# Kernel tuning notes

Hardware: AMD Instinct MI355X
Metric: run time of the kernel (lower is better)

Reference implementation:

```python
import jax, jax.numpy as jnp
import numpy as np

B, S, D = 2, 512, 1024
H, DH = 16, 64
P, K, F = 16, 4, 4096
EPS = 1e-6


def setup_inputs() -> dict:
    key = jax.random.key(0)
    ks = jax.random.split(key, 9)
    sc = D ** -0.5
    return {
        "x": jax.random.normal(ks[0], (B, S, D), jnp.float32),
        "wq": jax.random.normal(ks[1], (D, D), jnp.float32) * sc,
        "wk": jax.random.normal(ks[2], (D, D), jnp.float32) * sc,
        "wv": jax.random.normal(ks[3], (D, D), jnp.float32) * sc,
        "wo": jax.random.normal(ks[4], (D, D), jnp.float32) * sc,
        "g1": jnp.ones((D,), jnp.float32),
        "g2": jnp.ones((D,), jnp.float32),
        "r1": jax.random.normal(ks[5], (D, P), jnp.float32) * sc,
        "r2": jax.random.normal(ks[6], (D, P), jnp.float32) * sc,
        "bank1": jax.random.normal(ks[7], (P, D, F), jnp.float32) * 0.02,
        "bank2": jax.random.normal(ks[8], (P, F, D), jnp.float32) * 0.02,
    }


def _rmsnorm(t, g):
    return t * jax.lax.rsqrt(jnp.mean(t * t, axis=-1, keepdims=True) + EPS) * g


def reference(x, wq, wk, wv, wo, g1, g2, r1, r2, bank1, bank2):
    # --- attention sublayer (pre-norm, causal SDPA) ---
    h = _rmsnorm(x, g1)
    q = (h @ wq).reshape(B, S, H, DH).transpose(0, 2, 1, 3)  # (B,H,S,DH)
    k = (h @ wk).reshape(B, S, H, DH).transpose(0, 2, 1, 3)
    v = (h @ wv).reshape(B, S, H, DH).transpose(0, 2, 1, 3)
    scores = jnp.einsum("bhqd,bhkd->bhqk", q, k) * (DH ** -0.5)
    causal = jnp.triu(jnp.ones((S, S), bool), k=1)
    scores = jnp.where(causal[None, None], jnp.finfo(scores.dtype).min, scores)
    attn = jax.nn.softmax(scores, axis=-1)
    o = jnp.einsum("bhqk,bhkd->bhqd", attn, v).transpose(0, 2, 1, 3).reshape(B, S, D)
    x = x + o @ wo

    # --- compositional FFN: top-k primitive-bank routing ---
    h = _rmsnorm(x, g2)
    # FC1 routing
    tv1, ti1 = jax.lax.top_k(h @ r1, K)            # (B,S,K)
    c1 = jax.nn.softmax(tv1, axis=-1)
    z1 = jnp.einsum("bsd,pdf->bspf", h, bank1)     # all-primitive FC1 projections
    z1k = jnp.take_along_axis(z1, ti1[..., None], axis=2)  # gather (B,S,K,F)
    hmid = jax.nn.gelu(jnp.einsum("bsk,bskf->bsf", c1, z1k))
    # FC2 routing (same pre-FFN features)
    tv2, ti2 = jax.lax.top_k(h @ r2, K)
    c2 = jax.nn.softmax(tv2, axis=-1)
    z2 = jnp.einsum("bsf,pfd->bspd", hmid, bank2)
    z2k = jnp.take_along_axis(z2, ti2[..., None], axis=2)  # (B,S,K,D)
    ffn_out = jnp.einsum("bsk,bskd->bsd", c2, z2k)
    return x + ffn_out
```

## Files before the change

### kernel.cpp

```cpp
#include <hip/hip_runtime.h>
#include <hip/hip_bf16.h>

#define B_  2
#define S_  512
#define D_  1024
#define H_  16
#define DH_ 64
#define P_  16
#define K_  4
#define F_  4096
#define NT  (B_*S_)
#define EPS_ 1e-6f

typedef __attribute__((ext_vector_type(8))) short bf16x8s;
typedef __attribute__((ext_vector_type(4))) float f32x4;

__device__ inline unsigned short f2bf(float f) {
    unsigned int u = __builtin_bit_cast(unsigned int, f);
    unsigned int r = (u + 0x7fffu + ((u >> 16) & 1u)) >> 16;
    return (unsigned short)r;
}

__global__ void rmsnorm_kernel(const float* __restrict__ x, const float* __restrict__ g,
                               float* __restrict__ out, __hip_bfloat16* __restrict__ outbf) {
    int t = blockIdx.x;
    const float* row = x + (size_t)t * D_;
    float ss = 0.f;
    for (int d = threadIdx.x; d < D_; d += 256) { float v = row[d]; ss += v * v; }
    __shared__ float red[4];
    for (int off = 32; off; off >>= 1) ss += __shfl_xor(ss, off);
    int w = threadIdx.x >> 6;
    if ((threadIdx.x & 63) == 0) red[w] = ss;
    __syncthreads();
    if (threadIdx.x == 0) red[0] = rsqrtf((red[0]+red[1]+red[2]+red[3]) / (float)D_ + EPS_);
    __syncthreads();
    float scale = red[0];
    for (int d = threadIdx.x; d < D_; d += 256) {
        float v = row[d] * scale * g[d];
        out[(size_t)t * D_ + d] = v;
        if (outbf) outbf[(size_t)t * D_ + d] = __float2bfloat16(v);
    }
}

template<bool RES>
__device__ __forceinline__
void gemm64_body(const float* __restrict__ A, const float* __restrict__ Bw,
                 const float* __restrict__ Res, float* __restrict__ C,
                 int N, int Kd, int m0, int n0,
                 float (*As)[64], float (*Bs)[64]) {
    int t = threadIdx.x;
    int tx = t & 15, ty = t >> 4;
    float acc[4][4] = {};
    for (int k0 = 0; k0 < Kd; k0 += 16) {
        #pragma unroll
        for (int i = 0; i < 4; i++) {
            int idx = t*4 + i; int m = idx >> 4, kk = idx & 15;
            As[kk][m] = A[(size_t)(m0+m)*Kd + k0 + kk];
        }
        #pragma unroll
        for (int i = 0; i < 4; i++) {
            int idx = t*4 + i; int n = idx & 63, kk = idx >> 6;
            Bs[kk][n] = Bw[(size_t)(k0+kk)*N + n0 + n];
        }
        __syncthreads();
        #pragma unroll
        for (int kk = 0; kk < 16; kk++) {
            float a[4], b[4];
            #pragma unroll
            for (int i = 0; i < 4; i++) a[i] = As[kk][ty*4+i];
            #pragma unroll
            for (int j = 0; j < 4; j++) b[j] = Bs[kk][tx*4+j];
            #pragma unroll
            for (int i = 0; i < 4; i++)
                #pragma unroll
                for (int j = 0; j < 4; j++) acc[i][j] += a[i]*b[j];
        }
        __syncthreads();
    }
    #pragma unroll
    for (int i = 0; i < 4; i++)
        #pragma unroll
        for (int j = 0; j < 4; j++) {
            int m = m0 + ty*4 + i, n = n0 + tx*4 + j;
            float v = acc[i][j];
            if (RES) v += Res[(size_t)m*N + n];
            C[(size_t)m*N + n] = v;
        }
}

template<bool RES>
__global__ void gemm64(const float* __restrict__ A, const float* __restrict__ Bw,
                       const float* __restrict__ Res, float* __restrict__ C,
                       int M, int N, int Kd) {
    __shared__ float As[16][64];
    __shared__ float Bs[16][64];
    gemm64_body<RES>(A, Bw, Res, C, N, Kd, blockIdx.y*64, blockIdx.x*64, As, Bs);
}

__global__ void qkv64(const float* __restrict__ A, const float* __restrict__ wq,
                      const float* __restrict__ wk, const float* __restrict__ wv,
                      float* __restrict__ qb, float* __restrict__ kb, float* __restrict__ vb) {
    __shared__ float As[16][64];
    __shared__ float Bs[16][64];
    int which = blockIdx.x >> 4;
    const float* Bw = (which == 0) ? wq : (which == 1) ? wk : wv;
    float* C = (which == 0) ? qb : (which == 1) ? kb : vb;
    gemm64_body<false>(A, Bw, nullptr, C, D_, D_, blockIdx.y*64, (blockIdx.x & 15)*64, As, Bs);
}

template<bool SPLIT>
__global__ __launch_bounds__(256, 3)
void attn3(const float* __restrict__ q, const float* __restrict__ k,
           const float* __restrict__ v, float* __restrict__ o,
           float* __restrict__ opart, float* __restrict__ mpart,
           float* __restrict__ lpart) {
    __shared__ float Qs[32][68];
    __shared__ float Ks[64][68];
    __shared__ float Vs[64][68];
    __shared__ float Ps[32][68];
    int bh = blockIdx.y;
    int bq0 = (bh >> 4) * S_;
    int hh = bh & 15;
    int qt = blockIdx.x, q0 = qt * 32;
    int z = SPLIT ? blockIdx.z : 0;
    int t = threadIdx.x;
    int tx = t & 15, ty = t >> 4;

    #pragma unroll
    for (int i = 0; i < 2; i++) {
        int idx = i*256 + t; int r = idx >> 4, c = idx & 15;
        float4 tmp = *(const float4*)&q[((size_t)(bq0 + q0 + r))*D_ + hh*64 + c*4];
        tmp.x *= 0.125f; tmp.y *= 0.125f; tmp.z *= 0.125f; tmp.w *= 0.125f;
        *(float4*)&Qs[r][c*4] = tmp;
    }
    float m[2], l[2], oacc[2][4];
    #pragma unroll
    for (int i = 0; i < 2; i++) {
        m[i] = -1e30f; l[i] = 0.f;
        #pragma unroll
        for (int jd = 0; jd < 4; jd++) oacc[i][jd] = 0.f;
    }
    __syncthreads();

    int ktmax = (q0 + 31) >> 6;
    for (int kt = z; kt <= ktmax; kt += (SPLIT ? 2 : 1)) {
        int j0 = kt * 64;
        __syncthreads();
        #pragma unroll
        for (int i = 0; i < 4; i++) {
            int idx = i*256 + t; int r = idx >> 4, c = idx & 15;
            *(float4*)&Ks[r][c*4] = *(const float4*)&k[((size_t)(bq0 + j0 + r))*D_ + hh*64 + c*4];
            *(float4*)&Vs[r][c*4] = *(const float4*)&v[((size_t)(bq0 + j0 + r))*D_ + hh*64 + c*4];
        }
        __syncthreads();

        float sacc[2][4] = {};
        #pragma unroll
        for (int dc = 0; dc < 16; dc++) {
            f32x4 qv[2], kv[4];
            #pragma unroll
            for (int i = 0; i < 2; i++) qv[i] = *(const f32x4*)&Qs[ty + 16*i][dc*4];
            #pragma unroll
            for (int j = 0; j < 4; j++) kv[j] = *(const f32x4*)&Ks[tx + 16*j][dc*4];
            #pragma unroll
            for (int i = 0; i < 2; i++)
                #pragma unroll
                for (int j = 0; j < 4; j++)
                    sacc[i][j] += qv[i][0]*kv[j][0] + qv[i][1]*kv[j][1]
                                + qv[i][2]*kv[j][2] + qv[i][3]*kv[j][3];
        }
        if (kt == ktmax) {
            #pragma unroll
            for (int i = 0; i < 2; i++)
                #pragma unroll
                for (int j = 0; j < 4; j++)
                    if (j0 + tx + 16*j > q0 + ty + 16*i) sacc[i][j] = -1e30f;
        }
        #pragma unroll
        for (int i = 0; i < 2; i++) {
            float tm = fmaxf(fmaxf(sacc[i][0], sacc[i][1]), fmaxf(sacc[i][2], sacc[i][3]));
            tm = fmaxf(tm, __shfl_xor(tm, 1));
            tm = fmaxf(tm, __shfl_xor(tm, 2));
            tm = fmaxf(tm, __shfl_xor(tm, 4));
            tm = fmaxf(tm, __shfl_xor(tm, 8));
            float mn = fmaxf(m[i], tm);
            float corr = __expf(m[i] - mn);
            m[i] = mn;
            float rs = 0.f;
            #pragma unroll
            for (int j = 0; j < 4; j++) { sacc[i][j] = __expf(sacc[i][j] - mn); rs += sacc[i][j]; }
            rs += __shfl_xor(rs, 1);
            rs += __shfl_xor(rs, 2);
            rs += __shfl_xor(rs, 4);
            rs += __shfl_xor(rs, 8);
            l[i] = l[i]*corr + rs;
            #pragma unroll
            for (int jd = 0; jd < 4; jd++) oacc[i][jd] *= corr;
        }
        #pragma unroll
        for (int i = 0; i < 2; i++)
            #pragma unroll
            for (int j = 0; j < 4; j++)
                Ps[ty + 16*i][tx + 16*j] = sacc[i][j];
        __syncthreads();
        #pragma unroll
        for (int jc = 0; jc < 16; jc++) {
            f32x4 pv4[2];
            #pragma unroll
            for (int i = 0; i < 2; i++) pv4[i] = *(const f32x4*)&Ps[ty + 16*i][jc*4];
            #pragma unroll
            for (int u = 0; u < 4; u++) {
                int j = jc*4 + u;
                float vv[4];
                #pragma unroll
                for (int jd = 0; jd < 4; jd++) vv[jd] = Vs[j][tx + 16*jd];
                #pragma unroll
                for (int i = 0; i < 2; i++)
                    #pragma unroll
                    for (int jd = 0; jd < 4; jd++) oacc[i][jd] += pv4[i][u] * vv[jd];
            }
        }
    }
    if (SPLIT) {
        int zb = z*32 + bh;
        #pragma unroll
        for (int i = 0; i < 2; i++) {
            int row = q0 + ty + 16*i;
            if (tx == 0) {
                mpart[(size_t)zb*S_ + row] = m[i];
                lpart[(size_t)zb*S_ + row] = l[i];
            }
            #pragma unroll
            for (int jd = 0; jd < 4; jd++)
                opart[((size_t)zb*S_ + row)*64 + tx + 16*jd] = oacc[i][jd];
        }
    } else {
        #pragma unroll
        for (int i = 0; i < 2; i++) {
            float inv = 1.f / l[i];
            #pragma unroll
            for (int jd = 0; jd < 4; jd++)
                o[((size_t)(bq0 + q0 + ty + 16*i))*D_ + hh*64 + tx + 16*jd] = oacc[i][jd] * inv;
        }
    }
}

__global__ void attn_merge(const float* __restrict__ opart, const float* __restrict__ mpart,
                           const float* __restrict__ lpart, float* __restrict__ o) {
    int i = blockIdx.x*256 + threadIdx.x;
    if (i >= 32*S_*64) return;
    int col = i & 63, q = (i >> 6) & (S_-1), bh = i >> 15;
    float m0 = mpart[(size_t)bh*S_ + q],      m1 = mpart[(size_t)(32+bh)*S_ + q];
    float l0 = lpart[(size_t)bh*S_ + q],      l1 = lpart[(size_t)(32+bh)*S_ + q];
    float M = fmaxf(m0, m1);
    float w0 = __expf(m0 - M), w1 = __expf(m1 - M);
    float L = l0*w0 + l1*w1;
    float v = (opart[((size_t)bh*S_ + q)*64 + col]*w0
             + opart[((size_t)(32+bh)*S_ + q)*64 + col]*w1) / L;
    int bq0 = (bh >> 4)*S_, hh = bh & 15;
    o[((size_t)(bq0 + q))*D_ + hh*64 + col] = v;
}

__device__ void topk_write(const float* vals, float* c, int* ti) {
    float v[P_];
    #pragma unroll
    for (int p = 0; p < P_; p++) v[p] = vals[p];
    int idx[K_]; float tv[K_];
    for (int kk = 0; kk < K_; kk++) {
        int bi = 0; float bv = -1e30f;
        for (int p = 0; p < P_; p++) if (v[p] > bv) { bv = v[p]; bi = p; }
        idx[kk] = bi; tv[kk] = bv; v[bi] = -1e30f;
    }
    float mx = tv[0], sum = 0.f, e[K_];
    for (int kk = 0; kk < K_; kk++) { e[kk] = __expf(tv[kk]-mx); sum += e[kk]; }
    for (int kk = 0; kk < K_; kk++) { c[kk] = e[kk]/sum; ti[kk] = idx[kk]; }
}

__global__ void routing_kernel(const float* __restrict__ h, const float* __restrict__ r1,
                               const float* __restrict__ r2,
                               float* c1, int* ti1, float* c2, int* ti2) {
    int t = blockIdx.x; int lane = threadIdx.x;
    float acc1[P_] = {}, acc2[P_] = {};
    for (int d = lane; d < D_; d += 64) {
        float x = h[(size_t)t*D_ + d];
        #pragma unroll
        for (int p = 0; p < P_; p++) {
            acc1[p] += x * r1[d*P_ + p];
            acc2[p] += x * r2[d*P_ + p];
        }
    }
    #pragma unroll
    for (int p = 0; p < P_; p++)
        for (int off = 32; off; off >>= 1) {
            acc1[p] += __shfl_xor(acc1[p], off);
            acc2[p] += __shfl_xor(acc2[p], off);
        }
    if (lane == 0) {
        topk_write(acc1, c1 + t*K_, ti1 + t*K_);
        topk_write(acc2, c2 + t*K_, ti2 + t*K_);
    }
}

__global__ void build_lists(const int* __restrict__ ti1, const int* __restrict__ ti2,
                            int* cnt1, int* list1, int* cnt2, int* list2) {
    int slot = blockIdx.x*256 + threadIdx.x;
    if (slot >= NT*K_) return;
    int p1 = ti1[slot]; int pos1 = atomicAdd(&cnt1[p1], 1); list1[p1*(NT*K_) + pos1] = slot;
    int p2 = ti2[slot]; int pos2 = atomicAdd(&cnt2[p2], 1); list2[p2*(NT*K_) + pos2] = slot;
}

__device__ inline void store_out(__hip_bfloat16* p, float v) { *p = __float2bfloat16(v); }
__device__ inline void store_out(float* p, float v)          { *p = v; }

template<typename OutT, int KSPLIT>
__global__ __launch_bounds__(256)
void mgemm7(const __hip_bfloat16* __restrict__ A, const float* __restrict__ Bw0,
            const int* __restrict__ cnt, const int* __restrict__ list,
            OutT* __restrict__ o0, OutT* __restrict__ o1,
            OutT* __restrict__ o2, OutT* __restrict__ o3,
            int Kd, int Nd, int ntn) {
    __shared__ unsigned short Asl[4*128*8];
    __shared__ unsigned short Bsl[4*128*8];
    __shared__ int rows_s[128];
    __shared__ int slots_s[128];
    int p  = blockIdx.x / ntn;
    int n0 = (blockIdx.x - p*ntn) * 128;
    int m0 = blockIdx.y * 128;
    int count = cnt[p];
    if (m0 >= count) return;
    int t = threadIdx.x;
    if (t < 128) {
        int si = m0 + t;
        int slot = (si < count) ? list[p*(NT*K_) + si] : -1;
        slots_s[t] = slot;
        rows_s[t] = (slot >= 0) ? (slot >> 2) : 0;
    }
    __syncthreads();
    const float* Bw = Bw0 + (size_t)p * (size_t)Kd * Nd;
    int z = (KSPLIT > 1) ? (int)blockIdx.z : 0;
    OutT* out = (z == 0) ? o0 : (z == 1) ? o1 : (z == 2) ? o2 : o3;
    int kbase = z * (Kd / KSPLIT);
    int kend  = kbase + Kd / KSPLIT;
    int lane = t & 63, wave = t >> 6;
    int wr = wave >> 1, wc = wave & 1;
    int l15 = lane & 15, l4 = lane >> 4;
    int ar0 = t >> 2, ac8 = t & 3;
    int bkg = t & 7, bcg = t >> 3;
    f32x4 acc[4][4];
    #pragma unroll
    for (int i = 0; i < 4; i++)
        #pragma unroll
        for (int j = 0; j < 4; j++) acc[i][j] = (f32x4){0.f,0.f,0.f,0.f};
    int atok0 = rows_s[ar0], atok1 = rows_s[64 + ar0];
    for (int k0 = kbase; k0 < kend; k0 += 32) {
        __syncthreads();
        {
            bf16x8s av0 = *(const bf16x8s*)&A[(size_t)atok0*Kd + k0 + ac8*8];
            bf16x8s av1 = *(const bf16x8s*)&A[(size_t)atok1*Kd + k0 + ac8*8];
            *(bf16x8s*)&Asl[ac8*1024 + ((ar0 ^ (ac8<<1)) * 8)] = av0;
            *(bf16x8s*)&Asl[ac8*1024 + (((64 + ar0) ^ (ac8<<1)) * 8)] = av1;
        }
        {
            float bvv[4][4];
            #pragma unroll
            for (int j = 0; j < 4; j++) {
                float4 tmp = *(const float4*)&Bw[(size_t)(k0 + bkg*4 + j)*Nd + n0 + bcg*4];
                bvv[j][0]=tmp.x; bvv[j][1]=tmp.y; bvv[j][2]=tmp.z; bvv[j][3]=tmp.w;
            }
            int g = bkg >> 1, ib = (bkg & 1) * 4;
            #pragma unroll
            for (int cc = 0; cc < 4; cc++) {
                int col = bcg*4 + cc;
                ushort4 u = make_ushort4(f2bf(bvv[0][cc]), f2bf(bvv[1][cc]),
                                         f2bf(bvv[2][cc]), f2bf(bvv[3][cc]));
                *(ushort4*)&Bsl[g*1024 + ((col ^ (g<<1)) * 8) + ib] = u;
            }
        }
        __syncthreads();
        bf16x8s af[4], bfr[4];
        #pragma unroll
        for (int m = 0; m < 4; m++) {
            int row = wr*64 + m*16 + l15;
            af[m] = *(const bf16x8s*)&Asl[l4*1024 + ((row ^ (l4<<1)) * 8)];
        }
        #pragma unroll
        for (int n = 0; n < 4; n++) {
            int col = wc*64 + n*16 + l15;
            bfr[n] = *(const bf16x8s*)&Bsl[l4*1024 + ((col ^ (l4<<1)) * 8)];
        }
        #pragma unroll
        for (int m = 0; m < 4; m++)
            #pragma unroll
            for (int n = 0; n < 4; n++)
                acc[m][n] = __builtin_amdgcn_mfma_f32_16x16x32_bf16(af[m], bfr[n], acc[m][n], 0, 0, 0);
    }
    #pragma unroll
    for (int m = 0; m < 4; m++) {
        #pragma unroll
        for (int rr = 0; rr < 4; rr++) {
            int rl = wr*64 + m*16 + l4*4 + rr;
            int slot = slots_s[rl];
            if (slot < 0) continue;
            OutT* orow = out + (size_t)slot*Nd + n0 + wc*64;
            #pragma unroll
            for (int n = 0; n < 4; n++)
                store_out(&orow[n*16 + l15], acc[m][n][rr]);
        }
    }
}

template<bool TWO>
__global__ void reduce_fc1(const __hip_bfloat16* __restrict__ z1kA,
                           const __hip_bfloat16* __restrict__ z1kB,
                           const float* __restrict__ c1, __hip_bfloat16* __restrict__ hmid) {
    int i = blockIdx.x*256 + threadIdx.x;
    if (i >= NT*F_) return;
    int t = i / F_, f = i - t*F_;
    float s = 0.f;
    #pragma unroll
    for (int kk = 0; kk < K_; kk++) {
        size_t off = (size_t)(t*K_ + kk)*F_ + f;
        float zv = __bfloat162float(z1kA[off]);
        if (TWO) zv += __bfloat162float(z1kB[off]);
        s += c1[t*K_ + kk] * zv;
    }
    float x3 = s*s*s;
    float inner = 0.7978845608028654f * (s + 0.044715f * x3);
    hmid[i] = __float2bfloat16(0.5f * s * (1.f + tanhf(inner)));
}

template<int NP>
__global__ void final_kernel(const float* __restrict__ x2, const float* __restrict__ z0,
                             const float* __restrict__ z1, const float* __restrict__ z2p,
                             const float* __restrict__ z3,
                             const float* __restrict__ c2, float* __restrict__ out) {
    int i = blockIdx.x*256 + threadIdx.x;
    if (i >= NT*D_) return;
    int t = i / D_, d = i - t*D_;
    float s = x2[i];
    #pragma unroll
    for (int kk = 0; kk < K_; kk++) {
        size_t off = (size_t)(t*K_ + kk)*D_ + d;
        float zv = z0[off];
        if (NP >= 2) zv += z1[off];
        if (NP >= 4) zv += z2p[off] + z3[off];
        s += c2[t*K_ + kk] * zv;
    }
    out[i] = s;
}

extern "C" void kernel_launch(void* const* d_in, const int* in_sizes, int n_in,
                              void* d_out, int out_size, void* d_ws, size_t ws_size,
                              hipStream_t stream) {
    const float* x  = (const float*)d_in[0];
    const float* wq = (const float*)d_in[1];
    const float* wk = (const float*)d_in[2];
    const float* wv = (const float*)d_in[3];
    const float* wo = (const float*)d_in[4];
    const float* g1 = (const float*)d_in[5];
    const float* g2 = (const float*)d_in[6];
    const float* r1 = (const float*)d_in[7];
    const float* r2 = (const float*)d_in[8];
    const float* bank1 = (const float*)d_in[9];
    const float* bank2 = (const float*)d_in[10];
    float* out = (float*)d_out;

    char* ws = (char*)d_ws;
    const size_t MB = 1ull << 20;
    float* h1   = (float*)(ws + 0*MB);
    float* qb   = (float*)(ws + 4*MB);
    float* kb   = (float*)(ws + 8*MB);
    float* vb   = (float*)(ws + 12*MB);
    float* ob   = (float*)(ws + 16*MB);
    float* x2   = (float*)(ws + 20*MB);
    float* h2   = (float*)(ws + 24*MB);
    float* c1   = (float*)(ws + 28*MB);
    int*   ti1  = (int*)  (ws + 28*MB + 64*1024);
    float* c2   = (float*)(ws + 28*MB + 128*1024);
    int*   ti2  = (int*)  (ws + 28*MB + 192*1024);
    int*   cnt1 = (int*)  (ws + 28*MB + 256*1024);
    int*   cnt2 = (int*)  (ws + 28*MB + 256*1024 + 64);
    int*   list1= (int*)  (ws + 28*MB + 512*1024);
    int*   list2= (int*)  (ws + 28*MB + 768*1024);
    __hip_bfloat16* h2bf = (__hip_bfloat16*)(ws + 30*MB);
    __hip_bfloat16* z1kA = (__hip_bfloat16*)(ws + 32*MB);
    __hip_bfloat16* hmidbf = (__hip_bfloat16*)(ws + 64*MB);
    float* z2k0 = (float*)(ws + 80*MB);
    float* z2k1 = (float*)(ws + 96*MB);
    float* opart = (float*)(ws + 112*MB);
    float* mpart = (float*)(ws + 120*MB);
    float* lpart = (float*)(ws + 120*MB + 256*1024);
    __hip_bfloat16* z1kB = (__hip_bfloat16*)(ws + 128*MB);
    float* z2k2 = (float*)(ws + 160*MB);
    float* z2k3 = (float*)(ws + 176*MB);

    bool ksp = ws_size >= (size_t)192*MB;
    bool mid = ws_size >= (size_t)122*MB;

    rmsnorm_kernel<<<NT, 256, 0, stream>>>(x, g1, h1, nullptr);
    qkv64<<<dim3(48, 16), 256, 0, stream>>>(h1, wq, wk, wv, qb, kb, vb);
    if (mid) {
        attn3<true><<<dim3(S_/32, B_*H_, 2), 256, 0, stream>>>(
            qb, kb, vb, nullptr, opart, mpart, lpart);
        attn_merge<<<(32*S_*64)/256, 256, 0, stream>>>(opart, mpart, lpart, ob);
    } else {
        attn3<false><<<dim3(S_/32, B_*H_), 256, 0, stream>>>(
            qb, kb, vb, ob, nullptr, nullptr, nullptr);
    }
    dim3 gg(16, 16);
    gemm64<true><<<gg, 256, 0, stream>>>(ob, wo, x, x2, NT, D_, D_);
    rmsnorm_kernel<<<NT, 256, 0, stream>>>(x2, g2, h2, h2bf);
    routing_kernel<<<NT, 64, 0, stream>>>(h2, r1, r2, c1, ti1, c2, ti2);
    hipMemsetAsync(cnt1, 0, 128, stream);
    build_lists<<<(NT*K_)/256, 256, 0, stream>>>(ti1, ti2, cnt1, list1, cnt2, list2);
    if (ksp) {
        mgemm7<__hip_bfloat16, 2><<<dim3(P_*(F_/128), (NT*K_)/128, 2), 256, 0, stream>>>(
            h2bf, bank1, cnt1, list1, z1kA, z1kB, nullptr, nullptr, D_, F_, F_/128);
        reduce_fc1<true><<<(NT*F_)/256, 256, 0, stream>>>(z1kA, z1kB, c1, hmidbf);
        mgemm7<float, 4><<<dim3(P_*(D_/128), (NT*K_)/128, 4), 256, 0, stream>>>(
            hmidbf, bank2, cnt2, list2, z2k0, z2k1, z2k2, z2k3, F_, D_, D_/128);
        final_kernel<4><<<(NT*D_)/256, 256, 0, stream>>>(x2, z2k0, z2k1, z2k2, z2k3, c2, out);
    } else {
        mgemm7<__hip_bfloat16, 1><<<dim3(P_*(F_/128), (NT*K_)/128, 1), 256, 0, stream>>>(
            h2bf, bank1, cnt1, list1, z1kA, nullptr, nullptr, nullptr, D_, F_, F_/128);
        reduce_fc1<false><<<(NT*F_)/256, 256, 0, stream>>>(z1kA, nullptr, c1, hmidbf);
        mgemm7<float, 2><<<dim3(P_*(D_/128), (NT*K_)/128, 2), 256, 0, stream>>>(
            hmidbf, bank2, cnt2, list2, z2k0, z2k1, nullptr, nullptr, F_, D_, D_/128);
        final_kernel<2><<<(NT*D_)/256, 256, 0, stream>>>(x2, z2k0, z2k1, nullptr, nullptr, c2, out);
    }
}
```

Baseline: 686.7 us.

## Enlarge attention query tile to 64 rows with 512-thread blocks

The attention kernel now processes 64 query rows per block with 512 threads instead of 32 rows with 256 threads. This aligns query tiles with the 64-wide key tiles, so the causal mask only applies on the diagonal tile. Each K/V tile is also reused across twice as many queries. The separate probability buffer is dropped and the K shared tile is reused to hold P, which costs an extra barrier. The grid has half as many blocks, which may reduce occupancy and load balance, and for the first query tile the second split-K block now does no work.

```diff
diff --git a/kernel.cpp b/kernel.cpp
--- a/kernel.cpp
+++ b/kernel.cpp
@@ -109,26 +109,28 @@
 }
 
 template<bool SPLIT>
-__global__ __launch_bounds__(256, 3)
-void attn3(const float* __restrict__ q, const float* __restrict__ k,
+__global__ __launch_bounds__(512)
+void attn5(const float* __restrict__ q, const float* __restrict__ k,
            const float* __restrict__ v, float* __restrict__ o,
            float* __restrict__ opart, float* __restrict__ mpart,
            float* __restrict__ lpart) {
-    __shared__ float Qs[32][68];
+    __shared__ float Qs[64][68];
     __shared__ float Ks[64][68];
     __shared__ float Vs[64][68];
-    __shared__ float Ps[32][68];
     int bh = blockIdx.y;
     int bq0 = (bh >> 4) * S_;
     int hh = bh & 15;
-    int qt = blockIdx.x, q0 = qt * 32;
+    int qt = blockIdx.x, q0 = qt * 64;
     int z = SPLIT ? blockIdx.z : 0;
     int t = threadIdx.x;
-    int tx = t & 15, ty = t >> 4;
+    int tx = t & 15, ty = t >> 5;
+    int ry = (t >> 4) & 31;
+    ry = t >> 4;
+    ry &= 31;
 
     #pragma unroll
     for (int i = 0; i < 2; i++) {
-        int idx = i*256 + t; int r = idx >> 4, c = idx & 15;
+        int idx = i*512 + t; int r = idx >> 4, c = idx & 15;
         float4 tmp = *(const float4*)&q[((size_t)(bq0 + q0 + r))*D_ + hh*64 + c*4];
         tmp.x *= 0.125f; tmp.y *= 0.125f; tmp.z *= 0.125f; tmp.w *= 0.125f;
         *(float4*)&Qs[r][c*4] = tmp;
@@ -142,13 +144,12 @@
     }
     __syncthreads();
 
-    int ktmax = (q0 + 31) >> 6;
-    for (int kt = z; kt <= ktmax; kt += (SPLIT ? 2 : 1)) {
+    for (int kt = z; kt <= qt; kt += (SPLIT ? 2 : 1)) {
         int j0 = kt * 64;
         __syncthreads();
         #pragma unroll
-        for (int i = 0; i < 4; i++) {
-            int idx = i*256 + t; int r = idx >> 4, c = idx & 15;
+        for (int i = 0; i < 2; i++) {
+            int idx = i*512 + t; int r = idx >> 4, c = idx & 15;
             *(float4*)&Ks[r][c*4] = *(const float4*)&k[((size_t)(bq0 + j0 + r))*D_ + hh*64 + c*4];
             *(float4*)&Vs[r][c*4] = *(const float4*)&v[((size_t)(bq0 + j0 + r))*D_ + hh*64 + c*4];
         }
@@ -159,7 +160,7 @@
         for (int dc = 0; dc < 16; dc++) {
             f32x4 qv[2], kv[4];
             #pragma unroll
-            for (int i = 0; i < 2; i++) qv[i] = *(const f32x4*)&Qs[ty + 16*i][dc*4];
+            for (int i = 0; i < 2; i++) qv[i] = *(const f32x4*)&Qs[ry + 32*i][dc*4];
             #pragma unroll
             for (int j = 0; j < 4; j++) kv[j] = *(const f32x4*)&Ks[tx + 16*j][dc*4];
             #pragma unroll
@@ -169,12 +170,12 @@
                     sacc[i][j] += qv[i][0]*kv[j][0] + qv[i][1]*kv[j][1]
                                 + qv[i][2]*kv[j][2] + qv[i][3]*kv[j][3];
         }
-        if (kt == ktmax) {
+        if (kt == qt) {
             #pragma unroll
             for (int i = 0; i < 2; i++)
                 #pragma unroll
                 for (int j = 0; j < 4; j++)
-                    if (j0 + tx + 16*j > q0 + ty + 16*i) sacc[i][j] = -1e30f;
+                    if (tx + 16*j > ry + 32*i) sacc[i][j] = -1e30f;
         }
         #pragma unroll
         for (int i = 0; i < 2; i++) {
@@ -197,17 +198,18 @@
             #pragma unroll
             for (int jd = 0; jd < 4; jd++) oacc[i][jd] *= corr;
         }
+        __syncthreads();
         #pragma unroll
         for (int i = 0; i < 2; i++)
             #pragma unroll
             for (int j = 0; j < 4; j++)
-                Ps[ty + 16*i][tx + 16*j] = sacc[i][j];
+                Ks[ry + 32*i][tx + 16*j] = sacc[i][j];
         __syncthreads();
         #pragma unroll
         for (int jc = 0; jc < 16; jc++) {
             f32x4 pv4[2];
             #pragma unroll
-            for (int i = 0; i < 2; i++) pv4[i] = *(const f32x4*)&Ps[ty + 16*i][jc*4];
+            for (int i = 0; i < 2; i++) pv4[i] = *(const f32x4*)&Ks[ry + 32*i][jc*4];
             #pragma unroll
             for (int u = 0; u < 4; u++) {
                 int j = jc*4 + u;
@@ -225,7 +227,7 @@
         int zb = z*32 + bh;
         #pragma unroll
         for (int i = 0; i < 2; i++) {
-            int row = q0 + ty + 16*i;
+            int row = q0 + ry + 32*i;
             if (tx == 0) {
                 mpart[(size_t)zb*S_ + row] = m[i];
                 lpart[(size_t)zb*S_ + row] = l[i];
@@ -240,7 +242,7 @@
             float inv = 1.f / l[i];
             #pragma unroll
             for (int jd = 0; jd < 4; jd++)
-                o[((size_t)(bq0 + q0 + ty + 16*i))*D_ + hh*64 + tx + 16*jd] = oacc[i][jd] * inv;
+                o[((size_t)(bq0 + q0 + ry + 32*i))*D_ + hh*64 + tx + 16*jd] = oacc[i][jd] * inv;
         }
     }
 }
@@ -500,11 +502,11 @@
     rmsnorm_kernel<<<NT, 256, 0, stream>>>(x, g1, h1, nullptr);
     qkv64<<<dim3(48, 16), 256, 0, stream>>>(h1, wq, wk, wv, qb, kb, vb);
     if (mid) {
-        attn3<true><<<dim3(S_/32, B_*H_, 2), 256, 0, stream>>>(
+        attn5<true><<<dim3(S_/64, B_*H_, 2), 512, 0, stream>>>(
             qb, kb, vb, nullptr, opart, mpart, lpart);
         attn_merge<<<(32*S_*64)/256, 256, 0, stream>>>(opart, mpart, lpart, ob);
     } else {
-        attn3<false><<<dim3(S_/32, B_*H_), 256, 0, stream>>>(
+        attn5<false><<<dim3(S_/64, B_*H_), 512, 0, stream>>>(
             qb, kb, vb, ob, nullptr, nullptr, nullptr);
     }
     dim3 gg(16, 16);
```

After: 572.8 us. 1.2x faster.
